# Performance work log

Hardware: AMD Instinct MI355X
Metric: run time of the kernel (lower is better)

The kernel has to match this reference:

```python
import jax, jax.numpy as jnp
import numpy as np

LN_EPS = 1e-5
NORM_EPS = 1e-12  # torch F.normalize default eps


def _layernorm(x, gamma, beta):
    mu = x.mean(axis=-1, keepdims=True)
    var = ((x - mu) ** 2).mean(axis=-1, keepdims=True)
    return (x - mu) * jax.lax.rsqrt(var + LN_EPS) * gamma + beta


def _l2norm(x, axis):
    n = jnp.sqrt((x ** 2).sum(axis=axis, keepdims=True))
    return x / jnp.maximum(n, NORM_EPS)


def setup_inputs() -> dict:
    key = jax.random.key(0)
    ks = jax.random.split(key, 4)
    B, N, D, E, S, H = 64, 256, 1024, 16, 16, 256
    x = jax.random.normal(ks[0], (B, N, D), dtype=jnp.float32)
    mu = jax.random.normal(ks[1], (D, E, S), dtype=jnp.float32) / np.sqrt(D)
    w1 = jax.random.normal(ks[2], (E, D, H), dtype=jnp.float32) * np.sqrt(2.0 / D)
    w2 = jax.random.normal(ks[3], (E, H, D), dtype=jnp.float32) * np.sqrt(2.0 / (H + D))
    return {
        'x': x,
        'ln_gamma': jnp.ones((D,), jnp.float32),
        'ln_beta': jnp.zeros((D,), jnp.float32),
        'mu': mu,
        'scale': jnp.ones((1,), jnp.float32),
        'w1': w1,
        'b1': jnp.zeros((E, H), jnp.float32),
        'w2': w2,
        'b2': jnp.zeros((E, D), jnp.float32),
    }


def reference(x, ln_gamma, ln_beta, mu, scale, w1, b1, w2, b2):
    B, N, D = x.shape
    _, E, S = mu.shape
    # LayerNorm then cosine-similarity logits (eval mode: no noise, no dropout)
    xn = _layernorm(x, ln_gamma, ln_beta)                      # [B,N,D]
    x_unit = _l2norm(xn, axis=-1)                              # [B,N,D]
    mu_unit = _l2norm(mu, axis=0)                              # [D,E,S]
    logits = jnp.einsum('bnd,des->bnes', x_unit * scale, mu_unit)  # [B,N,E,S]
    # dispatch: softmax over tokens n; combine: softmax over flattened slots (e,s)
    dispatch = jax.nn.softmax(logits, axis=1)                  # [B,N,E,S]
    combine = jax.nn.softmax(logits.reshape(B, N, E * S), axis=-1).reshape(B, N, E, S)
    # dispatch tokens to slots
    slot_in = jnp.einsum('bnd,bnes->besd', xn, dispatch)       # [B,E,S,D]
    # batched per-expert MLP (GELU exact, matches nn.GELU default)
    h = jax.nn.gelu(jnp.einsum('besd,edh->besh', slot_in, w1) + b1[None, :, None, :], approximate=False)
    slot_out = jnp.einsum('besh,ehd->besd', h, w2) + b2[None, :, None, :]
    # combine slots back to tokens
    out = jnp.einsum('besd,bnes->bnd', slot_out, combine)      # [B,N,D]
    return out
```

## Files before the change

### kernel.cpp

```cpp
#include <hip/hip_runtime.h>

#define DD 1024
#define NN 256
#define BB 64
#define EE 16
#define SS 16
#define HH 256
#define ES 256
#define BN 16384

typedef unsigned short u16;
typedef unsigned int u32;
typedef __attribute__((ext_vector_type(8))) short bf16x8;
typedef __attribute__((ext_vector_type(4))) float f32x4;

#define MFMA(a, b, c) __builtin_amdgcn_mfma_f32_16x16x32_bf16(a, b, c, 0, 0, 0)

__device__ __forceinline__ u16 f2b(float f) {
  union { float f; u32 i; } c; c.f = f;
  u32 i = c.i;
  u32 r = (i + 0x7FFFu + ((i >> 16) & 1u)) >> 16;
  return (u16)r;
}

__device__ __forceinline__ float bredsum(float v, float* red) {
  #pragma unroll
  for (int o = 32; o > 0; o >>= 1) v += __shfl_down(v, o, 64);
  __syncthreads();
  if ((threadIdx.x & 63) == 0) red[threadIdx.x >> 6] = v;
  __syncthreads();
  return red[0] + red[1] + red[2] + red[3];
}

__global__ __launch_bounds__(256) void k_stats(
    const float* __restrict__ x, const float* __restrict__ gamma,
    const float* __restrict__ beta, const float* __restrict__ scale,
    float* __restrict__ mean_, float* __restrict__ rstd_,
    float* __restrict__ fct_) {
  __shared__ float red[4];
  int bn = blockIdx.x, t = threadIdx.x;
  float4 u = ((const float4*)(x + (size_t)bn * DD))[t];
  float s = u.x + u.y + u.z + u.w;
  float ss = u.x * u.x + u.y * u.y + u.z * u.z + u.w * u.w;
  s = bredsum(s, red);
  ss = bredsum(ss, red);
  float mean = s * (1.0f / DD);
  float var = ss * (1.0f / DD) - mean * mean;
  float rstd = rsqrtf(var + 1e-5f);
  float4 g = ((const float4*)gamma)[t];
  float4 be = ((const float4*)beta)[t];
  float x0 = (u.x - mean) * rstd * g.x + be.x;
  float x1 = (u.y - mean) * rstd * g.y + be.y;
  float x2 = (u.z - mean) * rstd * g.z + be.z;
  float x3 = (u.w - mean) * rstd * g.w + be.w;
  float s2 = x0 * x0 + x1 * x1 + x2 * x2 + x3 * x3;
  s2 = bredsum(s2, red);
  float f = scale[0] / fmaxf(sqrtf(s2), 1e-12f);
  if (t == 0) { mean_[bn] = mean; rstd_[bn] = rstd; fct_[bn] = f; }
}

__global__ __launch_bounds__(256) void k_rmun(
    const float* __restrict__ mu, const float* __restrict__ gamma,
    const float* __restrict__ beta, float* __restrict__ rmun,
    float* __restrict__ c3, float* __restrict__ c4) {
  __shared__ float red[4];
  int es = blockIdx.x, t = threadIdx.x;
  float ss = 0.f, s3 = 0.f, s4 = 0.f;
  #pragma unroll
  for (int j = 0; j < 4; j++) {
    int d = t + j * 256;
    float v = mu[(size_t)d * ES + es];
    ss += v * v;
    s3 += gamma[d] * v;
    s4 += beta[d] * v;
  }
  ss = bredsum(ss, red);
  s3 = bredsum(s3, red);
  s4 = bredsum(s4, red);
  if (t == 0) {
    float r = 1.0f / fmaxf(sqrtf(ss), 1e-12f);
    rmun[es] = r;
    c3[es] = s3 * r;
    c4[es] = s4 * r;
  }
}

__global__ __launch_bounds__(256) void k_mut(
    const float* __restrict__ mu, const float* __restrict__ gamma,
    const float* __restrict__ rmun, u16* __restrict__ muT) {
  __shared__ u16 L[256 * 70];
  int t = threadIdx.x;
  int d0 = blockIdx.x * 64;
  float rm = rmun[t];
  for (int i = 0; i < 64; i++) {
    int d = d0 + i;
    float gv = gamma[d];
    L[t * 70 + i] = f2b(mu[(size_t)d * ES + t] * rm * gv);
  }
  __syncthreads();
  u32 buf[32];
  #pragma unroll
  for (int k2 = 0; k2 < 32; k2++)
    buf[k2] = *(const u32*)&L[t * 70 + k2 * 2];
  u16* dst = muT + (size_t)t * DD + d0;
  #pragma unroll
  for (int k4 = 0; k4 < 8; k4++) {
    uint4 o;
    o.x = buf[k4 * 4]; o.y = buf[k4 * 4 + 1];
    o.z = buf[k4 * 4 + 2]; o.w = buf[k4 * 4 + 3];
    *(uint4*)(dst + k4 * 8) = o;
  }
}

__global__ __launch_bounds__(256) void k_xt(
    const float* __restrict__ x, u16* __restrict__ xT) {
  __shared__ u16 L[256 * 70];
  int t = threadIdx.x;
  int bn0 = blockIdx.x * 64;
  for (int cch = 0; cch < 4; cch++) {
    __syncthreads();
    for (int r = 0; r < 64; r++)
      L[t * 70 + r] = f2b(x[(size_t)(bn0 + r) * DD + cch * 256 + t]);
    __syncthreads();
    u32 buf[32];
    #pragma unroll
    for (int k2 = 0; k2 < 32; k2++)
      buf[k2] = *(const u32*)&L[t * 70 + k2 * 2];
    u16* dst = xT + (size_t)(cch * 256 + t) * BN + bn0;
    #pragma unroll
    for (int k4 = 0; k4 < 8; k4++) {
      uint4 o;
      o.x = buf[k4 * 4]; o.y = buf[k4 * 4 + 1];
      o.z = buf[k4 * 4 + 2]; o.w = buf[k4 * 4 + 3];
      *(uint4*)(dst + k4 * 8) = o;
    }
  }
}

__global__ __launch_bounds__(256) void k_tr(
    const float* __restrict__ src, u16* __restrict__ dst, int R, int C) {
  __shared__ u16 T[64 * 70];
  int t = threadIdx.x;
  int e = blockIdx.y;
  int tR = R >> 6;
  int r0 = (blockIdx.x % tR) * 64;
  int c0 = (blockIdx.x / tR) * 64;
  #pragma unroll
  for (int i = 0; i < 16; i++) {
    int r = r0 + i * 4 + (t >> 6);
    int c = t & 63;
    T[c * 70 + i * 4 + (t >> 6)] = f2b(src[((size_t)e * R + r) * C + c0 + c]);
  }
  __syncthreads();
  int cl = t >> 2, rsg = (t & 3) * 16;
  u32 buf[8];
  #pragma unroll
  for (int k2 = 0; k2 < 8; k2++)
    buf[k2] = *(const u32*)&T[cl * 70 + rsg + k2 * 2];
  u16* dp = dst + ((size_t)e * C + c0 + cl) * R + r0 + rsg;
  uint4 o0, o1;
  o0.x = buf[0]; o0.y = buf[1]; o0.z = buf[2]; o0.w = buf[3];
  o1.x = buf[4]; o1.y = buf[5]; o1.z = buf[6]; o1.w = buf[7];
  *(uint4*)dp = o0;
  *(uint4*)(dp + 8) = o1;
}

__global__ __launch_bounds__(256) void k_logits_mfma(
    const float* __restrict__ x, const u16* __restrict__ muT,
    const float* __restrict__ mean_, const float* __restrict__ rstd_,
    const float* __restrict__ fct_, const float* __restrict__ c3,
    const float* __restrict__ c4, float* __restrict__ logitsT) {
  __shared__ u16 xb[64 * 136];
  int t = threadIdx.x;
  int lane = t & 63, w = t >> 6, q = lane >> 4, m16 = lane & 15;
  int bn0 = blockIdx.x * 64;
  int es0 = w * 64;
  f32x4 z = {0.f, 0.f, 0.f, 0.f};
  f32x4 acc[4][4];
  #pragma unroll
  for (int mt = 0; mt < 4; mt++)
    #pragma unroll
    for (int nt = 0; nt < 4; nt++) acc[mt][nt] = z;
  int sr = t >> 5, cc = (t & 31) * 4;
  float4 pf[8];
  #pragma unroll
  for (int it = 0; it < 8; it++)
    pf[it] = *(const float4*)(x + (size_t)(bn0 + sr + it * 8) * DD + cc);
  for (int kb = 0; kb < 8; kb++) {
    __syncthreads();
    #pragma unroll
    for (int it = 0; it < 8; it++) {
      int row = sr + it * 8;
      uint2 pk;
      pk.x = (u32)f2b(pf[it].x) | ((u32)f2b(pf[it].y) << 16);
      pk.y = (u32)f2b(pf[it].z) | ((u32)f2b(pf[it].w) << 16);
      *(uint2*)&xb[row * 136 + cc] = pk;
    }
    __syncthreads();
    if (kb < 7) {
      #pragma unroll
      for (int it = 0; it < 8; it++)
        pf[it] = *(const float4*)(x + (size_t)(bn0 + sr + it * 8) * DD +
                                  (kb + 1) * 128 + cc);
    }
    #pragma unroll
    for (int ks = 0; ks < 4; ks++) {
      int k = ks * 32 + q * 8;
      bf16x8 a[4];
      #pragma unroll
      for (int mt = 0; mt < 4; mt++)
        a[mt] = *(const bf16x8*)(muT + (size_t)(es0 + mt * 16 + m16) * DD +
                                 kb * 128 + k);
      #pragma unroll
      for (int nt = 0; nt < 4; nt++) {
        bf16x8 bb = *(const bf16x8*)&xb[(nt * 16 + m16) * 136 + k];
        #pragma unroll
        for (int mt = 0; mt < 4; mt++)
          acc[mt][nt] = MFMA(a[mt], bb, acc[mt][nt]);
      }
    }
  }
  #pragma unroll
  for (int nt = 0; nt < 4; nt++) {
    int bn = bn0 + nt * 16 + m16;
    float fv = fct_[bn], rv = rstd_[bn], mv = mean_[bn];
    #pragma unroll
    for (int mt = 0; mt < 4; mt++)
      #pragma unroll
      for (int i = 0; i < 4; i++) {
        int es = es0 + mt * 16 + q * 4 + i;
        float val = fv * (rv * acc[mt][nt][i] - rv * mv * c3[es] + c4[es]);
        logitsT[(size_t)es * BN + bn] = val;
      }
  }
}

__global__ __launch_bounds__(256) void k_disp(
    const float* __restrict__ logitsT, const float* __restrict__ mean_,
    const float* __restrict__ rstd_, u16* __restrict__ dispW,
    float* __restrict__ c1g) {
  int t = threadIdx.x;
  int e = blockIdx.x, b = blockIdx.y;
  int s = t >> 4, c = t & 15;
  const float* lrow = logitsT + (size_t)(e * 16 + s) * BN + b * 256 + c * 16;
  float lv[16];
  #pragma unroll
  for (int i2 = 0; i2 < 4; i2++) {
    float4 f = *(const float4*)(lrow + i2 * 4);
    lv[i2 * 4 + 0] = f.x; lv[i2 * 4 + 1] = f.y;
    lv[i2 * 4 + 2] = f.z; lv[i2 * 4 + 3] = f.w;
  }
  float mx = -1e30f;
  #pragma unroll
  for (int i = 0; i < 16; i++) mx = fmaxf(mx, lv[i]);
  #pragma unroll
  for (int o = 1; o < 16; o <<= 1) mx = fmaxf(mx, __shfl_xor(mx, o, 64));
  float sum = 0.f;
  #pragma unroll
  for (int i = 0; i < 16; i++) { lv[i] = __expf(lv[i] - mx); sum += lv[i]; }
  #pragma unroll
  for (int o = 1; o < 16; o <<= 1) sum += __shfl_xor(sum, o, 64);
  float inv = 1.0f / sum;
  float c1p = 0.f;
  u16 wp[16];
  #pragma unroll
  for (int i = 0; i < 16; i++) {
    int n = c * 16 + i;
    float wv = lv[i] * inv * rstd_[b * 256 + n];
    c1p += wv * mean_[b * 256 + n];
    wp[i] = f2b(wv);
  }
  #pragma unroll
  for (int o = 1; o < 16; o <<= 1) c1p += __shfl_xor(c1p, o, 64);
  if (c == 0) c1g[(b << 8) + e * 16 + s] = c1p;
  u16* drow = dispW + ((size_t)(b * 256 + e * 16 + s)) * 256 + c * 16;
  #pragma unroll
  for (int i2 = 0; i2 < 4; i2++) {
    uint2 pk;
    pk.x = (u32)wp[i2 * 4] | ((u32)wp[i2 * 4 + 1] << 16);
    pk.y = (u32)wp[i2 * 4 + 2] | ((u32)wp[i2 * 4 + 3] << 16);
    *(uint2*)(drow + i2 * 4) = pk;
  }
}

__global__ __launch_bounds__(256) void k_comb(float* __restrict__ logitsT) {
  __shared__ float red[4][64];
  int t = threadIdx.x;
  int l = t & 63, g = t >> 6;
  int bn = blockIdx.y * 256 + blockIdx.x * 64 + l;
  float* base = logitsT + (size_t)(g * 64) * BN + bn;
  float ev[64];
  float sum = 0.f;
  #pragma unroll
  for (int i = 0; i < 64; i++) {
    float e = __expf(base[(size_t)i * BN]);
    ev[i] = e;
    sum += e;
  }
  red[g][l] = sum;
  __syncthreads();
  float inv = 1.0f / (red[0][l] + red[1][l] + red[2][l] + red[3][l]);
  #pragma unroll
  for (int i = 0; i < 64; i++)
    base[(size_t)i * BN] = ev[i] * inv;
}

__global__ __launch_bounds__(256) void k_slotin(
    const u16* __restrict__ xT, const u16* __restrict__ dispW,
    const float* __restrict__ c1g, const float* __restrict__ gamma,
    const float* __restrict__ beta, u16* __restrict__ SI) {
  __shared__ u16 xb[128 * 264];
  int t = threadIdx.x;
  int lane = t & 63, w = t >> 6, q = lane >> 4, m16 = lane & 15;
  int d0 = blockIdx.x * 128, b = blockIdx.y;
  #pragma unroll
  for (int it = 0; it < 16; it++) {
    int c = it * 256 + t;
    int row = c >> 5, off = (c & 31) * 8;
    uint4 v = *(const uint4*)(xT + (size_t)(d0 + row) * BN + b * 256 + off);
    *(uint4*)&xb[row * 264 + off] = v;
  }
  __syncthreads();
  f32x4 z = {0.f, 0.f, 0.f, 0.f};
  f32x4 acc[4][8];
  #pragma unroll
  for (int mt = 0; mt < 4; mt++)
    #pragma unroll
    for (int nt = 0; nt < 8; nt++) acc[mt][nt] = z;
  int es0 = w * 64;
  for (int ks = 0; ks < 8; ks++) {
    int k = ks * 32 + q * 8;
    bf16x8 a[4];
    #pragma unroll
    for (int mt = 0; mt < 4; mt++)
      a[mt] = *(const bf16x8*)(dispW +
               ((size_t)(b * 256 + es0 + mt * 16 + m16)) * 256 + k);
    #pragma unroll
    for (int nt = 0; nt < 8; nt++) {
      bf16x8 bb = *(const bf16x8*)&xb[(nt * 16 + m16) * 264 + k];
      #pragma unroll
      for (int mt = 0; mt < 4; mt++) acc[mt][nt] = MFMA(a[mt], bb, acc[mt][nt]);
    }
  }
  float gv[8], bev[8];
  #pragma unroll
  for (int nt = 0; nt < 8; nt++) {
    int d = d0 + nt * 16 + m16;
    gv[nt] = gamma[d]; bev[nt] = beta[d];
  }
  #pragma unroll
  for (int mt = 0; mt < 4; mt++) {
    float c1[4];
    #pragma unroll
    for (int i = 0; i < 4; i++)
      c1[i] = c1g[(b << 8) + es0 + mt * 16 + q * 4 + i];
    #pragma unroll
    for (int nt = 0; nt < 8; nt++)
      #pragma unroll
      for (int i = 0; i < 4; i++)
        SI[((size_t)(w * 4 + mt) * 1024 + b * 16 + q * 4 + i) * DD + d0 +
           nt * 16 + m16] = f2b(gv[nt] * (acc[mt][nt][i] - c1[i]) + bev[nt]);
  }
}

__global__ __launch_bounds__(256) void k_mlp1(
    const u16* __restrict__ SI, const u16* __restrict__ w1T,
    const float* __restrict__ b1, u16* __restrict__ H) {
  __shared__ u16 At[64 * 72];
  __shared__ u16 Bt[64 * 72];
  int t = threadIdx.x;
  int lane = t & 63, w = t >> 6, q = lane >> 4, m16 = lane & 15;
  int nt0 = blockIdx.x * 64;
  int mt0 = blockIdx.y * 64;
  int e = blockIdx.z;
  int wm = (w & 1) * 32, wn = (w >> 1) * 32;
  f32x4 z = {0.f, 0.f, 0.f, 0.f};
  f32x4 acc[2][2];
  #pragma unroll
  for (int mt = 0; mt < 2; mt++)
    #pragma unroll
    for (int nt = 0; nt < 2; nt++) acc[mt][nt] = z;
  const u16* Ab = SI + ((size_t)e * 1024 + mt0) * DD;
  const u16* Bb = w1T + ((size_t)e * HH + nt0) * DD;
  int row = t >> 2, off = (t & 3) * 16;
  uint4 pa0, pa1, pb0, pb1;
  pa0 = *(const uint4*)(Ab + (size_t)row * DD + off);
  pa1 = *(const uint4*)(Ab + (size_t)row * DD + off + 8);
  pb0 = *(const uint4*)(Bb + (size_t)row * DD + off);
  pb1 = *(const uint4*)(Bb + (size_t)row * DD + off + 8);
  for (int kb = 0; kb < 16; kb++) {
    *(uint4*)&At[row * 72 + off] = pa0;
    *(uint4*)&At[row * 72 + off + 8] = pa1;
    *(uint4*)&Bt[row * 72 + off] = pb0;
    *(uint4*)&Bt[row * 72 + off + 8] = pb1;
    __syncthreads();
    if (kb < 15) {
      int k0 = (kb + 1) * 64;
      pa0 = *(const uint4*)(Ab + (size_t)row * DD + k0 + off);
      pa1 = *(const uint4*)(Ab + (size_t)row * DD + k0 + off + 8);
      pb0 = *(const uint4*)(Bb + (size_t)row * DD + k0 + off);
      pb1 = *(const uint4*)(Bb + (size_t)row * DD + k0 + off + 8);
    }
    #pragma unroll
    for (int kk = 0; kk < 2; kk++) {
      int k = kk * 32 + q * 8;
      bf16x8 a[2], bb[2];
      #pragma unroll
      for (int mt = 0; mt < 2; mt++)
        a[mt] = *(const bf16x8*)&At[(wm + mt * 16 + m16) * 72 + k];
      #pragma unroll
      for (int nt = 0; nt < 2; nt++)
        bb[nt] = *(const bf16x8*)&Bt[(wn + nt * 16 + m16) * 72 + k];
      #pragma unroll
      for (int mt = 0; mt < 2; mt++)
        #pragma unroll
        for (int nt = 0; nt < 2; nt++)
          acc[mt][nt] = MFMA(a[mt], bb[nt], acc[mt][nt]);
    }
    __syncthreads();
  }
  #pragma unroll
  for (int nt = 0; nt < 2; nt++) {
    int h = nt0 + wn + nt * 16 + m16;
    float b1v = b1[e * HH + h];
    #pragma unroll
    for (int mt = 0; mt < 2; mt++)
      #pragma unroll
      for (int i = 0; i < 4; i++) {
        float zz = acc[mt][nt][i] + b1v;
        int bs = mt0 + wm + mt * 16 + q * 4 + i;
        H[((size_t)e * 1024 + bs) * HH + h] =
            f2b(0.5f * zz * (1.0f + erff(zz * 0.70710678118654752f)));
      }
  }
}

__global__ __launch_bounds__(256) void k_mlp2(
    const u16* __restrict__ H, const u16* __restrict__ w2T,
    const float* __restrict__ b2, u16* __restrict__ SO) {
  __shared__ u16 At[128 * 72];
  __shared__ u16 Bt[128 * 72];
  int t = threadIdx.x;
  int lane = t & 63, w = t >> 6, q = lane >> 4, m16 = lane & 15;
  int nt0 = blockIdx.x * 128;
  int mt0 = blockIdx.y * 128;
  int e = blockIdx.z;
  int wm = (w & 1) * 64, wn = (w >> 1) * 64;
  f32x4 z = {0.f, 0.f, 0.f, 0.f};
  f32x4 acc[4][4];
  #pragma unroll
  for (int mt = 0; mt < 4; mt++)
    #pragma unroll
    for (int nt = 0; nt < 4; nt++) acc[mt][nt] = z;
  const u16* Ab = H + ((size_t)e * 1024 + mt0) * HH;
  const u16* Bb = w2T + ((size_t)e * DD + nt0) * HH;
  for (int kb = 0; kb < 4; kb++) {
    __syncthreads();
    #pragma unroll
    for (int it = 0; it < 4; it++) {
      int c = it * 256 + t;
      int row = c >> 3, off = (c & 7) * 8;
      *(uint4*)&At[row * 72 + off] =
          *(const uint4*)(Ab + (size_t)row * HH + kb * 64 + off);
      *(uint4*)&Bt[row * 72 + off] =
          *(const uint4*)(Bb + (size_t)row * HH + kb * 64 + off);
    }
    __syncthreads();
    #pragma unroll
    for (int kk = 0; kk < 2; kk++) {
      int k = kk * 32 + q * 8;
      bf16x8 a[4], bb[4];
      #pragma unroll
      for (int mt = 0; mt < 4; mt++)
        a[mt] = *(const bf16x8*)&At[(wm + mt * 16 + m16) * 72 + k];
      #pragma unroll
      for (int nt = 0; nt < 4; nt++)
        bb[nt] = *(const bf16x8*)&Bt[(wn + nt * 16 + m16) * 72 + k];
      #pragma unroll
      for (int mt = 0; mt < 4; mt++)
        #pragma unroll
        for (int nt = 0; nt < 4; nt++)
          acc[mt][nt] = MFMA(a[mt], bb[nt], acc[mt][nt]);
    }
  }
  #pragma unroll
  for (int nt = 0; nt < 4; nt++) {
    int d = nt0 + wn + nt * 16 + m16;
    float b2v = b2[e * DD + d];
    #pragma unroll
    for (int mt = 0; mt < 4; mt++)
      #pragma unroll
      for (int i = 0; i < 4; i++) {
        int bs = mt0 + wm + mt * 16 + q * 4 + i;
        SO[((size_t)e * 1024 + bs) * DD + d] = f2b(acc[mt][nt][i] + b2v);
      }
  }
}

__global__ __launch_bounds__(256) void k_out_mfma(
    const u16* __restrict__ slot_out, const float* __restrict__ logitsT,
    float* __restrict__ out) {
  __shared__ u16 comb[32 * 264];
  __shared__ u16 sot[64 * 264];
  int t = threadIdx.x;
  int lane = t & 63, w = t >> 6, q = lane >> 4, m16 = lane & 15;
  int id = blockIdx.x;
  int b = (id & 7) * 8 + ((id >> 3) & 7);
  int dc = id >> 6;
  {
    int es2 = (t & 127) * 2, dh = t >> 7;
    const u16* s0 = slot_out +
        ((size_t)((es2 >> 4) * 1024 + b * 16 + (es2 & 15))) * DD +
        dc * 64 + dh * 32;
    const u16* s1 = s0 + DD;
    #pragma unroll
    for (int k2 = 0; k2 < 8; k2++) {
      ushort4 r0 = *(const ushort4*)(s0 + k2 * 4);
      ushort4 r1 = *(const ushort4*)(s1 + k2 * 4);
      int dl = dh * 32 + k2 * 4;
      *(u32*)&sot[(dl + 0) * 264 + es2] = (u32)r0.x | ((u32)r1.x << 16);
      *(u32*)&sot[(dl + 1) * 264 + es2] = (u32)r0.y | ((u32)r1.y << 16);
      *(u32*)&sot[(dl + 2) * 264 + es2] = (u32)r0.z | ((u32)r1.z << 16);
      *(u32*)&sot[(dl + 3) * 264 + es2] = (u32)r0.w | ((u32)r1.w << 16);
    }
  }
  for (int nch = 0; nch < 8; nch++) {
    int n0 = nch * 32;
    __syncthreads();
    {
      int j = t & 31, ch = t >> 5;
      const float* base = logitsT + (size_t)(ch * 32) * BN + b * 256 + n0 + j;
      float lv[32];
      #pragma unroll
      for (int i = 0; i < 32; i++) lv[i] = base[(size_t)i * BN];
      #pragma unroll
      for (int i2 = 0; i2 < 8; i2++) {
        uint2 pk;
        pk.x = (u32)f2b(lv[i2 * 4]) | ((u32)f2b(lv[i2 * 4 + 1]) << 16);
        pk.y = (u32)f2b(lv[i2 * 4 + 2]) | ((u32)f2b(lv[i2 * 4 + 3]) << 16);
        *(uint2*)&comb[j * 264 + ch * 32 + i2 * 4] = pk;
      }
    }
    __syncthreads();
    f32x4 aA = {0.f, 0.f, 0.f, 0.f}, aB = {0.f, 0.f, 0.f, 0.f};
    #pragma unroll
    for (int ks = 0; ks < 8; ks++) {
      bf16x8 bb = *(const bf16x8*)&sot[(w * 16 + m16) * 264 + ks * 32 + q * 8];
      bf16x8 a0 = *(const bf16x8*)&comb[m16 * 264 + ks * 32 + q * 8];
      bf16x8 a1 = *(const bf16x8*)&comb[(16 + m16) * 264 + ks * 32 + q * 8];
      aA = MFMA(a0, bb, aA);
      aB = MFMA(a1, bb, aB);
    }
    int d = dc * 64 + w * 16 + m16;
    #pragma unroll
    for (int i = 0; i < 4; i++) {
      out[((size_t)b * NN + n0 + q * 4 + i) * DD + d] = aA[i];
      out[((size_t)b * NN + n0 + 16 + q * 4 + i) * DD + d] = aB[i];
    }
  }
}

extern "C" void kernel_launch(void* const* d_in, const int* in_sizes, int n_in,
                              void* d_out, int out_size, void* d_ws, size_t ws_size,
                              hipStream_t stream) {
  const float* x     = (const float*)d_in[0];
  const float* gamma = (const float*)d_in[1];
  const float* beta  = (const float*)d_in[2];
  const float* mu    = (const float*)d_in[3];
  const float* scale = (const float*)d_in[4];
  const float* w1    = (const float*)d_in[5];
  const float* b1    = (const float*)d_in[6];
  const float* w2    = (const float*)d_in[7];
  const float* b2    = (const float*)d_in[8];
  float* out = (float*)d_out;

  const size_t WS_NEED = 50531328;
  if (ws_size < WS_NEED) return;
  char* ws = (char*)d_ws;
  u16*   sislot  = (u16*)(ws);
  float* logitsT = (float*)(ws + 33554432);
  float* mean_   = (float*)(ws + 50331648);
  float* rstd_   = (float*)(ws + 50397184);
  float* fct_    = (float*)(ws + 50462720);
  float* rmun    = (float*)(ws + 50528256);
  float* c3      = (float*)(ws + 50529280);
  float* c4      = (float*)(ws + 50530304);

  char* sc = (char*)d_out;
  u16* xT    = (u16*)(sc);
  u16* w1T   = (u16*)(sc + 33554432);
  u16* w2T   = (u16*)(sc + 41943040);
  u16* dispW = (u16*)(sc + 50331648);
  u16* muT   = (u16*)(sc + 58720256);
  float* c1g = (float*)(sc + 59244544);
  u16* Hbuf  = (u16*)(sc + 58720256);

  k_stats<<<BN, 256, 0, stream>>>(x, gamma, beta, scale, mean_, rstd_, fct_);
  k_rmun<<<ES, 256, 0, stream>>>(mu, gamma, beta, rmun, c3, c4);
  k_mut<<<16, 256, 0, stream>>>(mu, gamma, rmun, muT);
  k_xt<<<BN / 64, 256, 0, stream>>>(x, xT);
  k_tr<<<dim3(64, EE), 256, 0, stream>>>(w1, w1T, DD, HH);
  k_tr<<<dim3(64, EE), 256, 0, stream>>>(w2, w2T, HH, DD);
  k_logits_mfma<<<BN / 64, 256, 0, stream>>>(x, muT, mean_, rstd_, fct_,
                                             c3, c4, logitsT);
  k_disp<<<dim3(EE, BB), 256, 0, stream>>>(logitsT, mean_, rstd_, dispW, c1g);
  k_comb<<<dim3(4, BB), 256, 0, stream>>>(logitsT);
  k_slotin<<<dim3(8, BB), 256, 0, stream>>>(xT, dispW, c1g, gamma, beta, sislot);
  k_mlp1<<<dim3(4, 16, EE), 256, 0, stream>>>(sislot, w1T, b1, Hbuf);
  k_mlp2<<<dim3(8, 8, EE), 256, 0, stream>>>(Hbuf, w2T, b2, sislot);
  k_out_mfma<<<dim3(1024), 256, 0, stream>>>(sislot, logitsT, out);
}
```

Measured before the change: 379.4 us.

## Shrink mlp2 tiles to 64x64, prefetch next K-slice, stage output through LDS

The second expert MLP GEMM now uses 64x64 output tiles instead of 128x128, which quadruples the grid to 4096 blocks and cuts per-thread accumulators. Global loads for the next K-slice go into registers while the current slice is in MFMA, overlapping memory latency with compute. The epilogue writes bf16 results into shared memory and then stores them as coalesced 16-byte vectors instead of scattered 2-byte stores. Smaller tiles lower operand reuse and raise total global traffic for H and w2.

```diff
diff --git a/kernel.cpp b/kernel.cpp
--- a/kernel.cpp
+++ b/kernel.cpp
@@ -438,63 +438,75 @@
 __global__ __launch_bounds__(256) void k_mlp2(
     const u16* __restrict__ H, const u16* __restrict__ w2T,
     const float* __restrict__ b2, u16* __restrict__ SO) {
-  __shared__ u16 At[128 * 72];
-  __shared__ u16 Bt[128 * 72];
+  __shared__ u16 At[64 * 72];
+  __shared__ u16 Bt[64 * 72];
   int t = threadIdx.x;
   int lane = t & 63, w = t >> 6, q = lane >> 4, m16 = lane & 15;
-  int nt0 = blockIdx.x * 128;
-  int mt0 = blockIdx.y * 128;
+  int nt0 = blockIdx.x * 64;
+  int mt0 = blockIdx.y * 64;
   int e = blockIdx.z;
-  int wm = (w & 1) * 64, wn = (w >> 1) * 64;
+  int wm = (w & 1) * 32, wn = (w >> 1) * 32;
   f32x4 z = {0.f, 0.f, 0.f, 0.f};
-  f32x4 acc[4][4];
-  #pragma unroll
-  for (int mt = 0; mt < 4; mt++)
-    #pragma unroll
-    for (int nt = 0; nt < 4; nt++) acc[mt][nt] = z;
+  f32x4 acc[2][2];
+  #pragma unroll
+  for (int mt = 0; mt < 2; mt++)
+    #pragma unroll
+    for (int nt = 0; nt < 2; nt++) acc[mt][nt] = z;
   const u16* Ab = H + ((size_t)e * 1024 + mt0) * HH;
   const u16* Bb = w2T + ((size_t)e * DD + nt0) * HH;
+  int row = t >> 2, off = (t & 3) * 16;
+  uint4 pa0, pa1, pb0, pb1;
+  pa0 = *(const uint4*)(Ab + (size_t)row * HH + off);
+  pa1 = *(const uint4*)(Ab + (size_t)row * HH + off + 8);
+  pb0 = *(const uint4*)(Bb + (size_t)row * HH + off);
+  pb1 = *(const uint4*)(Bb + (size_t)row * HH + off + 8);
   for (int kb = 0; kb < 4; kb++) {
-    __syncthreads();
-    #pragma unroll
-    for (int it = 0; it < 4; it++) {
-      int c = it * 256 + t;
-      int row = c >> 3, off = (c & 7) * 8;
-      *(uint4*)&At[row * 72 + off] =
-          *(const uint4*)(Ab + (size_t)row * HH + kb * 64 + off);
-      *(uint4*)&Bt[row * 72 + off] =
-          *(const uint4*)(Bb + (size_t)row * HH + kb * 64 + off);
-    }
-    __syncthreads();
+    *(uint4*)&At[row * 72 + off] = pa0;
+    *(uint4*)&At[row * 72 + off + 8] = pa1;
+    *(uint4*)&Bt[row * 72 + off] = pb0;
+    *(uint4*)&Bt[row * 72 + off + 8] = pb1;
+    __syncthreads();
+    if (kb < 3) {
+      int k0 = (kb + 1) * 64;
+      pa0 = *(const uint4*)(Ab + (size_t)row * HH + k0 + off);
+      pa1 = *(const uint4*)(Ab + (size_t)row * HH + k0 + off + 8);
+      pb0 = *(const uint4*)(Bb + (size_t)row * HH + k0 + off);
+      pb1 = *(const uint4*)(Bb + (size_t)row * HH + k0 + off + 8);
+    }
     #pragma unroll
     for (int kk = 0; kk < 2; kk++) {
       int k = kk * 32 + q * 8;
-      bf16x8 a[4], bb[4];
-      #pragma unroll
-      for (int mt = 0; mt < 4; mt++)
+      bf16x8 a[2], bb[2];
+      #pragma unroll
+      for (int mt = 0; mt < 2; mt++)
         a[mt] = *(const bf16x8*)&At[(wm + mt * 16 + m16) * 72 + k];
       #pragma unroll
-      for (int nt = 0; nt < 4; nt++)
+      for (int nt = 0; nt < 2; nt++)
         bb[nt] = *(const bf16x8*)&Bt[(wn + nt * 16 + m16) * 72 + k];
       #pragma unroll
-      for (int mt = 0; mt < 4; mt++)
+      for (int mt = 0; mt < 2; mt++)
         #pragma unroll
-        for (int nt = 0; nt < 4; nt++)
+        for (int nt = 0; nt < 2; nt++)
           acc[mt][nt] = MFMA(a[mt], bb[nt], acc[mt][nt]);
     }
-  }
-  #pragma unroll
-  for (int nt = 0; nt < 4; nt++) {
-    int d = nt0 + wn + nt * 16 + m16;
-    float b2v = b2[e * DD + d];
-    #pragma unroll
-    for (int mt = 0; mt < 4; mt++)
+    __syncthreads();
+  }
+  #pragma unroll
+  for (int nt = 0; nt < 2; nt++) {
+    int dl = wn + nt * 16 + m16;
+    float b2v = b2[e * DD + nt0 + dl];
+    #pragma unroll
+    for (int mt = 0; mt < 2; mt++)
       #pragma unroll
       for (int i = 0; i < 4; i++) {
-        int bs = mt0 + wm + mt * 16 + q * 4 + i;
-        SO[((size_t)e * 1024 + bs) * DD + d] = f2b(acc[mt][nt][i] + b2v);
+        int bl = wm + mt * 16 + q * 4 + i;
+        At[bl * 72 + dl] = f2b(acc[mt][nt][i] + b2v);
       }
   }
+  __syncthreads();
+  u16* dst = SO + ((size_t)e * 1024 + mt0 + row) * DD + nt0 + off;
+  *(uint4*)dst = *(const uint4*)&At[row * 72 + off];
+  *(uint4*)(dst + 8) = *(const uint4*)&At[row * 72 + off + 8];
 }
 
 __global__ __launch_bounds__(256) void k_out_mfma(
@@ -607,6 +619,6 @@
   k_comb<<<dim3(4, BB), 256, 0, stream>>>(logitsT);
   k_slotin<<<dim3(8, BB), 256, 0, stream>>>(xT, dispW, c1g, gamma, beta, sislot);
   k_mlp1<<<dim3(4, 16, EE), 256, 0, stream>>>(sislot, w1T, b1, Hbuf);
-  k_mlp2<<<dim3(8, 8, EE), 256, 0, stream>>>(Hbuf, w2T, b2, sislot);
+  k_mlp2<<<dim3(16, 16, EE), 256, 0, stream>>>(Hbuf, w2T, b2, sislot);
   k_out_mfma<<<dim3(1024), 256, 0, stream>>>(sislot, logitsT, out);
 }
```

Result: faster. 364.9 us (-3.8%).
